# Performance work log

Measured on AMD Instinct MI355X. Metric: run time of the kernel, lower is better.

Reference implementation:

```python
import math
import jax, jax.numpy as jnp
import numpy as np

VOCAB, D, H, L, DFF, MAXLEN, PAD = 32000, 512, 8, 6, 2048, 5000, 0
DK = D // H
EPS = 1e-5


def _positional_encoding(max_len, d_model):
    pos = np.arange(max_len, dtype=np.float32)[:, None]
    div = np.exp(np.arange(0, d_model, 2, dtype=np.float32) * (-math.log(10000.0) / d_model))
    pe = np.zeros((max_len, d_model), dtype=np.float32)
    pe[:, 0::2] = np.sin(pos * div)
    pe[:, 1::2] = np.cos(pos * div)
    return jnp.asarray(pe)


def setup_inputs() -> dict:
    key = jax.random.key(0)
    ks = jax.random.split(key, 16)
    B, S = 2, 2048
    src = jax.random.randint(ks[0], (B, S), 0, VOCAB)
    emb = jax.random.normal(ks[1], (VOCAB, D), jnp.float32) * (D ** -0.5)
    emb = emb.at[PAD].set(0.0)  # padding_idx row zeroed
    pe = _positional_encoding(MAXLEN, D)
    s = 0.02
    WQ = jax.random.normal(ks[2], (L, D, D), jnp.float32) * s
    WK = jax.random.normal(ks[3], (L, D, D), jnp.float32) * s
    WV = jax.random.normal(ks[4], (L, D, D), jnp.float32) * s
    WO = jax.random.normal(ks[5], (L, D, D), jnp.float32) * s
    W1 = jax.random.normal(ks[6], (L, D, DFF), jnp.float32) * s
    b1 = jnp.zeros((L, DFF), jnp.float32)
    W2 = jax.random.normal(ks[7], (L, DFF, D), jnp.float32) * s
    b2 = jnp.zeros((L, D), jnp.float32)
    ln1_s = jnp.ones((L, D), jnp.float32); ln1_b = jnp.zeros((L, D), jnp.float32)
    ln2_s = jnp.ones((L, D), jnp.float32); ln2_b = jnp.zeros((L, D), jnp.float32)
    fn_s = jnp.ones((D,), jnp.float32); fn_b = jnp.zeros((D,), jnp.float32)
    return dict(src=src, emb=emb, pe=pe, WQ=WQ, WK=WK, WV=WV, WO=WO,
                W1=W1, b1=b1, W2=W2, b2=b2, ln1_s=ln1_s, ln1_b=ln1_b,
                ln2_s=ln2_s, ln2_b=ln2_b, fn_s=fn_s, fn_b=fn_b)


def _layernorm(x, scale, bias):
    mu = jnp.mean(x, axis=-1, keepdims=True)
    var = jnp.mean(jnp.square(x - mu), axis=-1, keepdims=True)
    return (x - mu) * jax.lax.rsqrt(var + EPS) * scale + bias


def _encoder_forward(src, emb, pe, WQ, WK, WV, WO, W1, b1, W2, b2,
                     ln1_s, ln1_b, ln2_s, ln2_b, fn_s, fn_b):
    B, S = src.shape
    key_mask = (src != PAD)[:, None, None, :]  # [B,1,1,S] padding mask
    x = emb[src] * math.sqrt(D) + pe[:S]        # [B,S,D] (dropout=eval/off)
    for l in range(L):
        # --- pre-LN self-attention ---
        h = _layernorm(x, ln1_s[l], ln1_b[l])
        q = (h @ WQ[l]).reshape(B, S, H, DK).transpose(0, 2, 1, 3)
        k = (h @ WK[l]).reshape(B, S, H, DK).transpose(0, 2, 1, 3)
        v = (h @ WV[l]).reshape(B, S, H, DK).transpose(0, 2, 1, 3)
        scores = jnp.einsum('bhqd,bhkd->bhqk', q, k) / math.sqrt(DK)
        scores = jnp.where(key_mask, scores, -jnp.inf)
        w = jax.nn.softmax(scores, axis=-1)
        w = jnp.nan_to_num(w, nan=0.0)
        attn = jnp.einsum('bhqk,bhkd->bhqd', w, v)
        attn = attn.transpose(0, 2, 1, 3).reshape(B, S, D) @ WO[l]
        x = x + attn
        # --- pre-LN FFN ---
        h = _layernorm(x, ln2_s[l], ln2_b[l])
        h = jax.nn.relu(h @ W1[l] + b1[l]) @ W2[l] + b2[l]
        x = x + h
    return _layernorm(x, fn_s, fn_b)


def reference(src, emb, pe, WQ, WK, WV, WO, W1, b1, W2, b2,
              ln1_s, ln1_b, ln2_s, ln2_b, fn_s, fn_b):
    return _encoder_forward(src, emb, pe, WQ, WK, WV, WO, W1, b1, W2, b2,
                            ln1_s, ln1_b, ln2_s, ln2_b, fn_s, fn_b)
```

## Files before the change

kernel.cpp:

```cpp
#include <hip/hip_runtime.h>


typedef _Float16 f16;
typedef _Float16 f16x8 __attribute__((ext_vector_type(8)));
typedef _Float16 f16x4 __attribute__((ext_vector_type(4)));
typedef float    f32x4 __attribute__((ext_vector_type(4)));

#define MFMA16(a, b, c) __builtin_amdgcn_mfma_f32_16x16x32_f16((a), (b), (c), 0, 0, 0)
#define GLOAD_LDS16(GP, LP)                                        \
  __builtin_amdgcn_global_load_lds(                                \
      (const __attribute__((address_space(1))) void*)(GP),         \
      (__attribute__((address_space(3))) void*)(LP), 16, 0, 0)

__device__ inline float fast_exp2(float x) {
#if __has_builtin(__builtin_amdgcn_exp2f)
  return __builtin_amdgcn_exp2f(x);
#else
  return exp2f(x);
#endif
}

static constexpr int Dm  = 512;
static constexpr int Sx  = 2048;
static constexpr int NTOK = 4096;
static constexpr int DFFm = 2048;
static constexpr int Lc  = 6;

__global__ __launch_bounds__(256) void transpose_cvt(
    const float* __restrict__ in, f16* __restrict__ out, int R, int C)
{
  __shared__ float t[32][33];
  const int z = blockIdx.z;
  const float* src = in + (size_t)z * R * C;
  f16* dst = out + (size_t)z * R * C;
  const int r0 = blockIdx.y * 32, c0 = blockIdx.x * 32;
  const int tx = threadIdx.x, ty = threadIdx.y;
  #pragma unroll
  for (int i = 0; i < 4; i++)
    t[ty + i * 8][tx] = src[(size_t)(r0 + ty + i * 8) * C + c0 + tx];
  __syncthreads();
  #pragma unroll
  for (int i = 0; i < 4; i++)
    dst[(size_t)(c0 + ty + i * 8) * R + r0 + tx] = (f16)t[tx][ty + i * 8];
}

__global__ __launch_bounds__(256) void embed_k(
    const int* __restrict__ src, const float* __restrict__ emb,
    const float* __restrict__ pe, float* __restrict__ x)
{
  const int gid = blockIdx.x * 256 + threadIdx.x;
  const int token = gid >> 6;
  const int d0 = (gid & 63) << 3;
  const int s = token & (Sx - 1);
  const int tk = src[token];
  const float* e = emb + (size_t)tk * Dm + d0;
  const float* p = pe + (size_t)s * Dm + d0;
  float* o = x + (size_t)token * Dm + d0;
  const float SC = 22.627416997969522f;
  #pragma unroll
  for (int j = 0; j < 8; j++) o[j] = e[j] * SC + p[j];
}

__global__ __launch_bounds__(256) void mask_k(
    const int* __restrict__ src, float* __restrict__ mb)
{
  const int i = blockIdx.x * 256 + threadIdx.x;
  mb[i] = (src[i] != 0) ? 0.f : -3.0e38f;
}

template <typename OUT>
__global__ __launch_bounds__(256) void ln_k(
    const float* __restrict__ x, const float* __restrict__ sc,
    const float* __restrict__ bi, OUT* __restrict__ out)
{
  const int row = blockIdx.x * 4 + (threadIdx.x >> 6);
  const int l = threadIdx.x & 63;
  const float* px = x + (size_t)row * Dm + l * 8;
  float v[8];
  *(float4*)&v[0] = *(const float4*)px;
  *(float4*)&v[4] = *(const float4*)(px + 4);
  float s = 0.f;
  #pragma unroll
  for (int j = 0; j < 8; j++) s += v[j];
  #pragma unroll
  for (int m = 1; m < 64; m <<= 1) s += __shfl_xor(s, m);
  const float mu = s * (1.0f / 512.0f);
  float qv = 0.f;
  #pragma unroll
  for (int j = 0; j < 8; j++) { float d = v[j] - mu; qv += d * d; }
  #pragma unroll
  for (int m = 1; m < 64; m <<= 1) qv += __shfl_xor(qv, m);
  const float inv = rsqrtf(qv * (1.0f / 512.0f) + 1e-5f);
  float scv[8], biv[8];
  *(float4*)&scv[0] = *(const float4*)(sc + l * 8);
  *(float4*)&scv[4] = *(const float4*)(sc + l * 8 + 4);
  *(float4*)&biv[0] = *(const float4*)(bi + l * 8);
  *(float4*)&biv[4] = *(const float4*)(bi + l * 8 + 4);
  if constexpr (sizeof(OUT) == 2) {
    f16x8 o;
    #pragma unroll
    for (int j = 0; j < 8; j++) o[j] = (f16)((v[j] - mu) * inv * scv[j] + biv[j]);
    *(f16x8*)((f16*)out + (size_t)row * Dm + l * 8) = o;
  } else {
    float o[8];
    #pragma unroll
    for (int j = 0; j < 8; j++) o[j] = (v[j] - mu) * inv * scv[j] + biv[j];
    float* po = (float*)out + (size_t)row * Dm + l * 8;
    *(float4*)po = *(float4*)&o[0];
    *(float4*)(po + 4) = *(float4*)&o[4];
  }
}

template <int BN, int MODE, int N, int K>
__global__ __launch_bounds__(256) void gemm_k(
    const f16* __restrict__ A,
    const f16* __restrict__ B0, const f16* __restrict__ B1, const f16* __restrict__ B2,
    f16* __restrict__ O0, f16* __restrict__ O1, f16* __restrict__ O2,
    float* __restrict__ xio, const float* __restrict__ bias)
{
  constexpr int BM = 128;
  constexpr int NF = (BN >= 32) ? (BN / 32) : 1;
  constexpr int NBM = NTOK / BM;
  constexpr int NBN = N / BN;
  constexpr int NZ = (MODE == 0) ? 3 : 1;
  constexpr int NB = NBM * NBN * NZ;
  __shared__ f16 lsA[BM * 64];
  __shared__ f16 lsB[BN * 64];
  const int tid = threadIdx.x;
  const int l = tid & 63, w = tid >> 6;
  const int lr = l & 15, lh = l >> 4;
  const int wm = w >> 1, wn = w & 1;
  const int bid = blockIdx.x;
  const int nid = (bid & 7) * (NB / 8) + (bid >> 3);
  const int z = nid / (NBM * NBN);
  const int rr = nid % (NBM * NBN);
  const int bm = rr / NBN, bn = rr % NBN;
  const f16* Bt = (z == 0) ? B0 : ((z == 1) ? B1 : B2);
  f16* Oz = (z == 0) ? O0 : O1;

  constexpr int ACH = (BM * 64) / (256 * 8);
  constexpr int BCH = (BN * 64) / (256 * 8);
  const size_t rowA0 = (size_t)bm * BM;
  const size_t rowB0 = (size_t)bn * BN;

  f32x4 acc[4][NF] = {};
  constexpr int NT = K >> 6;
  for (int kt = 0; kt < NT; ++kt) {
    __syncthreads();
    #pragma unroll
    for (int i = 0; i < ACH; i++) {
      int c = i * 256 + tid;
      GLOAD_LDS16(A + (rowA0 + (c >> 3)) * K + kt * 64 + (c & 7) * 8, lsA + c * 8);
    }
    #pragma unroll
    for (int i = 0; i < BCH; i++) {
      int c = i * 256 + tid;
      GLOAD_LDS16(Bt + (rowB0 + (c >> 3)) * K + kt * 64 + (c & 7) * 8, lsB + c * 8);
    }
    __syncthreads();
    #pragma unroll
    for (int s = 0; s < 2; s++) {
      f16x8 af[4], bf[NF];
      #pragma unroll
      for (int mf = 0; mf < 4; mf++)
        af[mf] = *(const f16x8*)(lsA + (wm * 64 + mf * 16 + lr) * 64 + s * 32 + lh * 8);
      #pragma unroll
      for (int nf = 0; nf < NF; nf++)
        bf[nf] = *(const f16x8*)(lsB + (wn * (BN / 2) + nf * 16 + lr) * 64 + s * 32 + lh * 8);
      #pragma unroll
      for (int mf = 0; mf < 4; mf++)
        #pragma unroll
        for (int nf = 0; nf < NF; nf++)
          acc[mf][nf] = MFMA16(af[mf], bf[nf], acc[mf][nf]);
    }
  }

  #pragma unroll
  for (int mf = 0; mf < 4; mf++) {
    #pragma unroll
    for (int nf = 0; nf < NF; nf++) {
      const int token = bm * BM + wm * 64 + mf * 16 + lh * 4;
      const int ch = bn * BN + wn * (BN / 2) + nf * 16 + lr;
      if constexpr (MODE == 0) {
        if (z == 2) {
          f16x4 o;
          #pragma unroll
          for (int r = 0; r < 4; r++) o[r] = (f16)acc[mf][nf][r];
          const int bb = token >> 11, ss = token & (Sx - 1);
          *(f16x4*)(O2 + ((size_t)((bb << 3) + (ch >> 6)) * 64 + (ch & 63)) * Sx + ss) = o;
        } else {
          #pragma unroll
          for (int r = 0; r < 4; r++)
            Oz[(size_t)(token + r) * N + ch] = (f16)acc[mf][nf][r];
        }
      } else {
        #pragma unroll
        for (int r = 0; r < 4; r++) {
          float v = acc[mf][nf][r];
          size_t idx = (size_t)(token + r) * N + ch;
          if constexpr (MODE == 1) {
            xio[idx] += v;
          } else if constexpr (MODE == 2) {
            v += bias[ch];
            O0[idx] = (f16)fmaxf(v, 0.f);
          } else {
            xio[idx] += v + bias[ch];
          }
        }
      }
    }
  }
}

__global__ __launch_bounds__(512) void attn_k(
    const f16* __restrict__ q, const f16* __restrict__ kk,
    const f16* __restrict__ vt, const float* __restrict__ maskb,
    f16* __restrict__ out)
{
  __shared__ f16 lsK[2][2][64 * 64];
  __shared__ f16 lsV[2][2][64 * 64];
  const int tid = threadIdx.x;
  const int l = tid & 63, w = tid >> 6;
  const int lr = l & 15, lh = l >> 4;
  const int grp = w >> 2;
  const int t256 = tid & 255;
  const int bid = blockIdx.x;
  const int nid = ((bid & 7) << 6) + (bid >> 3);
  const int bh = nid >> 5;
  const int qt = nid & 31;
  const int b = bh >> 3, h = bh & 7;

  const _Float16 QS = (_Float16)0.18033688f;
  f16x8 qf[2];
  #pragma unroll
  for (int s = 0; s < 2; s++) {
    size_t row = (size_t)(b * Sx + qt * 64 + (w & 3) * 16 + lr);
    f16x8 t = *(const f16x8*)(q + row * Dm + h * 64 + s * 32 + lh * 8);
    qf[s] = t * QS;
  }

  f32x4 oacc[4] = {};
  float mrun = -1e30f;
  float lrun = 0.f;

  auto stage = [&](int t, int pb) {
    #pragma unroll
    for (int i = 0; i < 2; i++) {
      int c = i * 256 + t256, r = c >> 3, g = c & 7, gs = g ^ (r & 7);
      GLOAD_LDS16(kk + (size_t)(b * Sx + t * 64 + r) * Dm + h * 64 + gs * 8,
                  &lsK[grp][pb][c * 8]);
      GLOAD_LDS16(vt + (size_t)(bh * 64 + r) * Sx + t * 64 + gs * 8,
                  &lsV[grp][pb][c * 8]);
    }
  };
  stage(grp * 16, 0);

  for (int i = 0; i < 16; ++i) {
    const int t = grp * 16 + i;
    const int cur = i & 1;
    __syncthreads();
    if (i < 15) stage(t + 1, cur ^ 1);

    f32x4 sacc[4];
    #pragma unroll
    for (int kf = 0; kf < 4; kf++)
      sacc[kf] = *(const f32x4*)(maskb + b * Sx + t * 64 + kf * 16 + lh * 4);
    __builtin_amdgcn_s_setprio(1);
    #pragma unroll
    for (int s = 0; s < 2; s++) {
      const int gk = (s * 4 + lh) ^ (lr & 7);
      #pragma unroll
      for (int kf = 0; kf < 4; kf++) {
        f16x8 a = *(const f16x8*)(&lsK[grp][cur][(kf * 16 + lr) * 64 + gk * 8]);
        sacc[kf] = MFMA16(a, qf[s], sacc[kf]);
      }
    }
    __builtin_amdgcn_s_setprio(0);

    float pmax = -3.0e38f;
    #pragma unroll
    for (int kf = 0; kf < 4; kf++)
      #pragma unroll
      for (int r = 0; r < 4; r++) pmax = fmaxf(pmax, sacc[kf][r]);
    pmax = fmaxf(pmax, __shfl_xor(pmax, 16));
    pmax = fmaxf(pmax, __shfl_xor(pmax, 32));
    if (!__all(pmax - mrun <= 8.0f)) {
      const float mnew = fmaxf(mrun, pmax);
      const float rs = fast_exp2(mrun - mnew);
      lrun *= rs;
      #pragma unroll
      for (int mf = 0; mf < 4; mf++) oacc[mf] *= rs;
      mrun = mnew;
    }
    float ps = 0.f;
    f16x8 pa[2];
    #pragma unroll
    for (int kf = 0; kf < 4; kf++)
      #pragma unroll
      for (int r = 0; r < 4; r++) {
        float p = fast_exp2(sacc[kf][r] - mrun);
        sacc[kf][r] = p;
        ps += p;
      }
    ps += __shfl_xor(ps, 16);
    ps += __shfl_xor(ps, 32);
    lrun += ps;
    #pragma unroll
    for (int s = 0; s < 2; s++)
      #pragma unroll
      for (int jj = 0; jj < 8; jj++)
        pa[s][jj] = (f16)sacc[2 * s + (jj >> 2)][jj & 3];

    __builtin_amdgcn_s_setprio(1);
    #pragma unroll
    for (int s = 0; s < 2; s++) {
      const int g0 = (s * 4 + (lh >> 1)) ^ (lr & 7);
      const int g1 = ((s * 4 + (lh >> 1)) + 2) ^ (lr & 7);
      #pragma unroll
      for (int mf = 0; mf < 4; mf++) {
        union { f16x8 v8; f16x4 v4[2]; } u;
        const f16* vbase = &lsV[grp][cur][(mf * 16 + lr) * 64];
        u.v4[0] = *(const f16x4*)(vbase + g0 * 8 + (lh & 1) * 4);
        u.v4[1] = *(const f16x4*)(vbase + g1 * 8 + (lh & 1) * 4);
        oacc[mf] = MFMA16(u.v8, pa[s], oacc[mf]);
      }
    }
    __builtin_amdgcn_s_setprio(0);
  }

  __syncthreads();
  float* sO  = (float*)&lsK[0][0][0];
  float* sML = (float*)&lsV[0][0][0];
  const int wl = (w & 3) * 64 + l;
  if (grp == 1) {
    #pragma unroll
    for (int mf = 0; mf < 4; mf++)
      #pragma unroll
      for (int r = 0; r < 4; r++) sO[wl * 16 + mf * 4 + r] = oacc[mf][r];
    sML[wl * 2] = mrun;
    sML[wl * 2 + 1] = lrun;
  }
  __syncthreads();
  if (grp == 0) {
    const float m1 = sML[wl * 2], l1 = sML[wl * 2 + 1];
    const float mm = fmaxf(mrun, m1);
    const float s0 = fast_exp2(mrun - mm), s1 = fast_exp2(m1 - mm);
    const float inv = 1.f / (lrun * s0 + l1 * s1);
    size_t row = (size_t)(b * Sx + qt * 64 + (w & 3) * 16 + lr);
    #pragma unroll
    for (int mf = 0; mf < 4; mf++) {
      f16x4 o;
      #pragma unroll
      for (int r = 0; r < 4; r++)
        o[r] = (f16)((oacc[mf][r] * s0 + sO[wl * 16 + mf * 4 + r] * s1) * inv);
      *(f16x4*)(out + row * Dm + h * 64 + mf * 16 + lh * 4) = o;
    }
  }
}

extern "C" void kernel_launch(void* const* d_in, const int* in_sizes, int n_in,
                              void* d_out, int out_size, void* d_ws, size_t ws_size,
                              hipStream_t stream)
{
  (void)in_sizes; (void)n_in; (void)out_size; (void)ws_size;
  const int*   src  = (const int*)d_in[0];
  const float* emb  = (const float*)d_in[1];
  const float* pe   = (const float*)d_in[2];
  const float* WQ   = (const float*)d_in[3];
  const float* WK   = (const float*)d_in[4];
  const float* WV   = (const float*)d_in[5];
  const float* WO   = (const float*)d_in[6];
  const float* W1   = (const float*)d_in[7];
  const float* b1   = (const float*)d_in[8];
  const float* W2   = (const float*)d_in[9];
  const float* b2   = (const float*)d_in[10];
  const float* ln1s = (const float*)d_in[11];
  const float* ln1b = (const float*)d_in[12];
  const float* ln2s = (const float*)d_in[13];
  const float* ln2b = (const float*)d_in[14];
  const float* fns  = (const float*)d_in[15];
  const float* fnb  = (const float*)d_in[16];

  char* ws = (char*)d_ws;
  const size_t DD = (size_t)Dm * Dm;
  const size_t DF = (size_t)Dm * DFFm;
  f16* wtQ = (f16*)(ws);
  f16* wtK = wtQ + Lc * DD;
  f16* wtV = wtK + Lc * DD;
  f16* wtO = wtV + Lc * DD;
  f16* wt1 = wtO + Lc * DD;
  f16* wt2 = wt1 + Lc * DF;
  float* x  = (float*)(wt2 + Lc * DF);
  f16* hbuf = (f16*)(x + (size_t)NTOK * Dm);
  f16* qb   = hbuf + (size_t)NTOK * Dm;
  f16* kb   = qb + (size_t)NTOK * Dm;
  f16* vtb  = kb + (size_t)NTOK * Dm;
  f16* attn = vtb + (size_t)NTOK * Dm;
  f16* ff   = attn + (size_t)NTOK * Dm;
  float* maskb = (float*)(ff + (size_t)NTOK * DFFm);

  const dim3 tb(32, 8);
  transpose_cvt<<<dim3(16, 16, Lc), tb, 0, stream>>>(WQ, wtQ, Dm, Dm);
  transpose_cvt<<<dim3(16, 16, Lc), tb, 0, stream>>>(WK, wtK, Dm, Dm);
  transpose_cvt<<<dim3(16, 16, Lc), tb, 0, stream>>>(WV, wtV, Dm, Dm);
  transpose_cvt<<<dim3(16, 16, Lc), tb, 0, stream>>>(WO, wtO, Dm, Dm);
  transpose_cvt<<<dim3(64, 16, Lc), tb, 0, stream>>>(W1, wt1, Dm, DFFm);
  transpose_cvt<<<dim3(16, 64, Lc), tb, 0, stream>>>(W2, wt2, DFFm, Dm);

  embed_k<<<1024, 256, 0, stream>>>(src, emb, pe, x);
  mask_k<<<16, 256, 0, stream>>>(src, maskb);

  for (int l = 0; l < Lc; l++) {
    const f16* wq = wtQ + (size_t)l * DD;
    const f16* wk = wtK + (size_t)l * DD;
    const f16* wv = wtV + (size_t)l * DD;
    const f16* wo = wtO + (size_t)l * DD;
    const f16* w1 = wt1 + (size_t)l * DF;
    const f16* w2 = wt2 + (size_t)l * DF;

    ln_k<f16><<<1024, 256, 0, stream>>>(x, ln1s + l * Dm, ln1b + l * Dm, hbuf);
    gemm_k<64, 0, 512, 512><<<768, 256, 0, stream>>>(
        hbuf, wq, wk, wv, qb, kb, vtb, nullptr, nullptr);
    attn_k<<<512, 512, 0, stream>>>(qb, kb, vtb, maskb, attn);
    gemm_k<32, 1, 512, 512><<<512, 256, 0, stream>>>(
        attn, wo, wo, wo, nullptr, nullptr, nullptr, x, nullptr);
    ln_k<f16><<<1024, 256, 0, stream>>>(x, ln2s + l * Dm, ln2b + l * Dm, hbuf);
    gemm_k<128, 2, 2048, 512><<<512, 256, 0, stream>>>(
        hbuf, w1, w1, w1, ff, ff, ff, nullptr, b1 + (size_t)l * DFFm);
    gemm_k<32, 3, 512, 2048><<<512, 256, 0, stream>>>(
        ff, w2, w2, w2, nullptr, nullptr, nullptr, x, b2 + (size_t)l * Dm);
  }

  ln_k<float><<<1024, 256, 0, stream>>>(x, fns, fnb, (float*)d_out);
}
```

Before: 742.7 us.

## Double-buffer GEMM LDS tiles, permute V layout, compute softmax sums via MFMA

The GEMM kernel now double-buffers its A/B LDS tiles, prefetching the next K-tile while the current one is computed, and drops one barrier per iteration. The V-transpose store permutes sequence columns so the attention kernel can read V with a single 16-byte LDS load instead of two 8-byte loads. The attention kernel computes row sums of P with an MFMA against a ones vector, replacing cross-lane shuffle reductions, and rebalances the max reduction into a tree. This doubles GEMM LDS use, which may reduce occupancy, and the sums now come from f16-rounded probabilities.

```diff
diff --git a/kernel.cpp b/kernel.cpp
--- a/kernel.cpp
+++ b/kernel.cpp
@@ -119,13 +119,13 @@
     float* __restrict__ xio, const float* __restrict__ bias)
 {
   constexpr int BM = 128;
-  constexpr int NF = (BN >= 32) ? (BN / 32) : 1;
+  constexpr int NF = BN / 32;
   constexpr int NBM = NTOK / BM;
   constexpr int NBN = N / BN;
   constexpr int NZ = (MODE == 0) ? 3 : 1;
   constexpr int NB = NBM * NBN * NZ;
-  __shared__ f16 lsA[BM * 64];
-  __shared__ f16 lsB[BN * 64];
+  __shared__ f16 lsA[2][BM * 64];
+  __shared__ f16 lsB[2][BN * 64];
   const int tid = threadIdx.x;
   const int l = tid & 63, w = tid >> 6;
   const int lr = l & 15, lh = l >> 4;
@@ -143,30 +143,35 @@
   const size_t rowA0 = (size_t)bm * BM;
   const size_t rowB0 = (size_t)bn * BN;
 
+  auto stage = [&](int kt, int pb) {
+    #pragma unroll
+    for (int i = 0; i < ACH; i++) {
+      int c = i * 256 + tid;
+      GLOAD_LDS16(A + (rowA0 + (c >> 3)) * K + kt * 64 + (c & 7) * 8, &lsA[pb][c * 8]);
+    }
+    #pragma unroll
+    for (int i = 0; i < BCH; i++) {
+      int c = i * 256 + tid;
+      GLOAD_LDS16(Bt + (rowB0 + (c >> 3)) * K + kt * 64 + (c & 7) * 8, &lsB[pb][c * 8]);
+    }
+  };
+
   f32x4 acc[4][NF] = {};
+  stage(0, 0);
   constexpr int NT = K >> 6;
   for (int kt = 0; kt < NT; ++kt) {
+    const int cur = kt & 1;
     __syncthreads();
-    #pragma unroll
-    for (int i = 0; i < ACH; i++) {
-      int c = i * 256 + tid;
-      GLOAD_LDS16(A + (rowA0 + (c >> 3)) * K + kt * 64 + (c & 7) * 8, lsA + c * 8);
-    }
-    #pragma unroll
-    for (int i = 0; i < BCH; i++) {
-      int c = i * 256 + tid;
-      GLOAD_LDS16(Bt + (rowB0 + (c >> 3)) * K + kt * 64 + (c & 7) * 8, lsB + c * 8);
-    }
-    __syncthreads();
+    if (kt + 1 < NT) stage(kt + 1, cur ^ 1);
     #pragma unroll
     for (int s = 0; s < 2; s++) {
       f16x8 af[4], bf[NF];
       #pragma unroll
       for (int mf = 0; mf < 4; mf++)
-        af[mf] = *(const f16x8*)(lsA + (wm * 64 + mf * 16 + lr) * 64 + s * 32 + lh * 8);
+        af[mf] = *(const f16x8*)(&lsA[cur][(wm * 64 + mf * 16 + lr) * 64 + s * 32 + lh * 8]);
       #pragma unroll
       for (int nf = 0; nf < NF; nf++)
-        bf[nf] = *(const f16x8*)(lsB + (wn * (BN / 2) + nf * 16 + lr) * 64 + s * 32 + lh * 8);
+        bf[nf] = *(const f16x8*)(&lsB[cur][(wn * (BN / 2) + nf * 16 + lr) * 64 + s * 32 + lh * 8]);
       #pragma unroll
       for (int mf = 0; mf < 4; mf++)
         #pragma unroll
@@ -187,7 +192,8 @@
           #pragma unroll
           for (int r = 0; r < 4; r++) o[r] = (f16)acc[mf][nf][r];
           const int bb = token >> 11, ss = token & (Sx - 1);
-          *(f16x4*)(O2 + ((size_t)((bb << 3) + (ch >> 6)) * 64 + (ch & 63)) * Sx + ss) = o;
+          const int scol = (ss & ~31) | (((ss >> 2) & 3) << 3) | (((ss >> 4) & 1) << 2);
+          *(f16x4*)(O2 + ((size_t)((bb << 3) + (ch >> 6)) * 64 + (ch & 63)) * Sx + scol) = o;
         } else {
           #pragma unroll
           for (int r = 0; r < 4; r++)
@@ -239,9 +245,11 @@
     qf[s] = t * QS;
   }
 
+  const f16x8 ones = {(f16)1, (f16)1, (f16)1, (f16)1,
+                      (f16)1, (f16)1, (f16)1, (f16)1};
   f32x4 oacc[4] = {};
+  f32x4 sumacc = {};
   float mrun = -1e30f;
-  float lrun = 0.f;
 
   auto stage = [&](int t, int pb) {
     #pragma unroll
@@ -277,57 +285,55 @@
     }
     __builtin_amdgcn_s_setprio(0);
 
-    float pmax = -3.0e38f;
-    #pragma unroll
-    for (int kf = 0; kf < 4; kf++)
-      #pragma unroll
-      for (int r = 0; r < 4; r++) pmax = fmaxf(pmax, sacc[kf][r]);
+    float pmax;
+    {
+      float t0 = fmaxf(fmaxf(sacc[0][0], sacc[0][1]), sacc[0][2]);
+      float t1 = fmaxf(fmaxf(sacc[0][3], sacc[1][0]), sacc[1][1]);
+      float t2 = fmaxf(fmaxf(sacc[1][2], sacc[1][3]), sacc[2][0]);
+      float t3 = fmaxf(fmaxf(sacc[2][1], sacc[2][2]), sacc[2][3]);
+      float t4 = fmaxf(fmaxf(sacc[3][0], sacc[3][1]), sacc[3][2]);
+      float u0 = fmaxf(fmaxf(t0, t1), sacc[3][3]);
+      float u1 = fmaxf(fmaxf(t2, t3), t4);
+      pmax = fmaxf(u0, u1);
+    }
     pmax = fmaxf(pmax, __shfl_xor(pmax, 16));
     pmax = fmaxf(pmax, __shfl_xor(pmax, 32));
     if (!__all(pmax - mrun <= 8.0f)) {
       const float mnew = fmaxf(mrun, pmax);
       const float rs = fast_exp2(mrun - mnew);
-      lrun *= rs;
+      sumacc *= rs;
       #pragma unroll
       for (int mf = 0; mf < 4; mf++) oacc[mf] *= rs;
       mrun = mnew;
     }
-    float ps = 0.f;
+    #pragma unroll
+    for (int kf = 0; kf < 4; kf++)
+      #pragma unroll
+      for (int r = 0; r < 4; r++)
+        sacc[kf][r] = fast_exp2(sacc[kf][r] - mrun);
     f16x8 pa[2];
-    #pragma unroll
-    for (int kf = 0; kf < 4; kf++)
-      #pragma unroll
-      for (int r = 0; r < 4; r++) {
-        float p = fast_exp2(sacc[kf][r] - mrun);
-        sacc[kf][r] = p;
-        ps += p;
-      }
-    ps += __shfl_xor(ps, 16);
-    ps += __shfl_xor(ps, 32);
-    lrun += ps;
     #pragma unroll
     for (int s = 0; s < 2; s++)
       #pragma unroll
       for (int jj = 0; jj < 8; jj++)
         pa[s][jj] = (f16)sacc[2 * s + (jj >> 2)][jj & 3];
+    sumacc = MFMA16(ones, pa[0], sumacc);
+    sumacc = MFMA16(ones, pa[1], sumacc);
 
     __builtin_amdgcn_s_setprio(1);
     #pragma unroll
     for (int s = 0; s < 2; s++) {
-      const int g0 = (s * 4 + (lh >> 1)) ^ (lr & 7);
-      const int g1 = ((s * 4 + (lh >> 1)) + 2) ^ (lr & 7);
+      const int gv = (4 * s + lh) ^ (lr & 7);
       #pragma unroll
       for (int mf = 0; mf < 4; mf++) {
-        union { f16x8 v8; f16x4 v4[2]; } u;
-        const f16* vbase = &lsV[grp][cur][(mf * 16 + lr) * 64];
-        u.v4[0] = *(const f16x4*)(vbase + g0 * 8 + (lh & 1) * 4);
-        u.v4[1] = *(const f16x4*)(vbase + g1 * 8 + (lh & 1) * 4);
-        oacc[mf] = MFMA16(u.v8, pa[s], oacc[mf]);
+        f16x8 vv = *(const f16x8*)(&lsV[grp][cur][(mf * 16 + lr) * 64 + gv * 8]);
+        oacc[mf] = MFMA16(vv, pa[s], oacc[mf]);
       }
     }
     __builtin_amdgcn_s_setprio(0);
   }
 
+  const float lrun = sumacc[0];
   __syncthreads();
   float* sO  = (float*)&lsK[0][0][0];
   float* sML = (float*)&lsV[0][0][0];
```

Result: no change. 734.9 us (-1.1%).
